# Optimization experiments

Measured on AMD Instinct MI355X. Metric: run time of the kernel, lower is better.

Reference implementation:

```python
import jax, jax.numpy as jnp
import numpy as np

MAT_MODE = [(0, 1), (0, 2), (1, 2)]   # plane axes per component (TensoRF VM)
VEC_MODE = [2, 1, 0]                  # line axis per component
DISTANCE_SCALE = 1.0
WHITE_BG = True


def _bilinear(plane, uv):
    """plane: [C,H,W]; uv: [P,2] in [-1,1] (uv[:,0]->W, uv[:,1]->H). align_corners=True."""
    H, W = plane.shape[-2], plane.shape[-1]
    x = (uv[:, 0] + 1.0) * 0.5 * (W - 1)
    y = (uv[:, 1] + 1.0) * 0.5 * (H - 1)
    x0 = jnp.clip(jnp.floor(x), 0, W - 2).astype(jnp.int32)
    y0 = jnp.clip(jnp.floor(y), 0, H - 2).astype(jnp.int32)
    wx = x - x0
    wy = y - y0
    v00 = plane[:, y0, x0]
    v01 = plane[:, y0, x0 + 1]
    v10 = plane[:, y0 + 1, x0]
    v11 = plane[:, y0 + 1, x0 + 1]
    top = v00 * (1 - wx) + v01 * wx
    bot = v10 * (1 - wx) + v11 * wx
    return top * (1 - wy) + bot * wy   # [C,P]


def _linear1d(line, t):
    """line: [C,L]; t: [P] in [-1,1]. align_corners=True."""
    L = line.shape[-1]
    x = (t + 1.0) * 0.5 * (L - 1)
    x0 = jnp.clip(jnp.floor(x), 0, L - 2).astype(jnp.int32)
    w = x - x0
    return line[:, x0] * (1 - w) + line[:, x0 + 1] * w   # [C,P]


def setup_inputs() -> dict:
    key = jax.random.key(0)
    ks = jax.random.split(key, 8)
    N_rays = 4096
    # camera origins on a sphere of radius 4, dirs aimed at points inside the box
    o = jax.random.normal(ks[0], (N_rays, 3), jnp.float32)
    o = o / jnp.linalg.norm(o, axis=-1, keepdims=True) * 4.0
    tgt = jax.random.uniform(ks[1], (N_rays, 3), jnp.float32, -0.5, 0.5)
    d = tgt - o
    d = d / jnp.linalg.norm(d, axis=-1, keepdims=True)
    rays = jnp.concatenate([o, d], axis=-1)
    return {
        "rays": rays,
        "density_plane": 0.1 * jax.random.normal(ks[2], (3, 16, 256, 256), jnp.float32),
        "density_line": 0.1 * jax.random.normal(ks[3], (3, 16, 256), jnp.float32),
        "app_plane": 0.1 * jax.random.normal(ks[4], (3, 24, 256, 256), jnp.float32),
        "app_line": 0.1 * jax.random.normal(ks[5], (3, 24, 256), jnp.float32),
        "basis_mat": 0.1 * jax.random.normal(ks[6], (72, 3), jnp.float32),
        "aabb": jnp.array([[-1.5, -1.5, -1.5], [1.5, 1.5, 1.5]], jnp.float32),
        "N_samples": 256,
    }


def reference(rays, density_plane, density_line, app_plane, app_line, basis_mat, aabb, N_samples):
    N = rays.shape[0]
    o, d = rays[:, :3], rays[:, 3:6]
    # ray / aabb intersection
    vec = jnp.where(jnp.abs(d) < 1e-6, 1e-6, d)
    rate_a = (aabb[1] - o) / vec
    rate_b = (aabb[0] - o) / vec
    t_min = jnp.clip(jnp.minimum(rate_a, rate_b).max(-1), 0.05)
    t_max = jnp.maximum(jnp.maximum(rate_a, rate_b).min(-1), t_min + 1e-3)
    s = jnp.linspace(0.0, 1.0, N_samples, dtype=jnp.float32)
    z = t_min[:, None] * (1.0 - s) + t_max[:, None] * s          # [N,S]
    dists = jnp.diff(z, axis=-1)
    dists = jnp.concatenate([dists, dists[:, -1:]], axis=-1)      # [N,S]
    pts = o[:, None, :] + d[:, None, :] * z[..., None]            # [N,S,3]
    coords = (pts - aabb[0]) / (aabb[1] - aabb[0]) * 2.0 - 1.0
    inside = jnp.all(jnp.abs(coords) <= 1.0, axis=-1)             # [N,S]
    cf = coords.reshape(-1, 3)                                    # [P,3]

    sigma_feat = 0.0
    app_feats = []
    for i in range(3):
        uv = cf[:, list(MAT_MODE[i])]
        w = cf[:, VEC_MODE[i]]
        sigma_feat = sigma_feat + (_bilinear(density_plane[i], uv) * _linear1d(density_line[i], w)).sum(0)
        app_feats.append(_bilinear(app_plane[i], uv) * _linear1d(app_line[i], w))
    app = jnp.concatenate(app_feats, axis=0).T                    # [P, 72]

    sigma = jax.nn.softplus(sigma_feat).reshape(N, -1) * inside   # [N,S]
    alpha = 1.0 - jnp.exp(-sigma * dists * DISTANCE_SCALE)        # [N,S]
    T = jnp.cumprod(1.0 - alpha + 1e-10, axis=-1)
    T = jnp.concatenate([jnp.ones_like(T[:, :1]), T[:, :-1]], axis=-1)
    weights = alpha * T                                           # [N,S]

    rgb = jax.nn.sigmoid(app @ basis_mat).reshape(N, -1, 3)       # [N,S,3]
    rgb_map = (weights[..., None] * rgb).sum(1)                   # [N,3]
    acc = weights.sum(-1)
    if WHITE_BG:
        rgb_map = rgb_map + (1.0 - acc)[..., None]
    rgb_map = jnp.clip(rgb_map, 0.0, 1.0)
    depth_map = (weights * z).sum(-1, keepdims=True)              # [N,1]
    return rgb_map, depth_map
```

## Files before the change

### kernel.cpp

```cpp
#include <hip/hip_runtime.h>
#include <hip/hip_fp16.h>
#include <cmath>

#define NRAYS 4096
#define NSAMP 256
#define NSAMPLES_TOT (NRAYS * NSAMP)

static constexpr size_t DPT_B = 0;
static constexpr size_t DLT_B = 3145728;
static constexpr size_t APT_B = DLT_B + 24576;
static constexpr size_t ALT_B = APT_B + 4718592;
static constexpr size_t SMP_B = ALT_B + 18432;
static constexpr size_t RAY_B = SMP_B + 8388608;
static constexpr size_t WS_NEED = RAY_B + 131072;

typedef _Float16 __attribute__((ext_vector_type(2))) v2h;
typedef __attribute__((ext_vector_type(2))) float f32x2;

struct u96 { unsigned x, y, z; };

__device__ __forceinline__ u96 ld12(const void* p) {
  u96 v;
  __builtin_memcpy(&v, p, 12);
  return v;
}

__device__ __forceinline__ float dot2acc(__half2 a, __half2 b, float c) {
  return __builtin_amdgcn_fdot2(__builtin_bit_cast(v2h, a),
                                __builtin_bit_cast(v2h, b), c, false);
}

__device__ __forceinline__ __half2 lerp2(__half2 a, __half2 b, __half2 w) {
  return __hfma2(w, __hsub2(b, a), a);
}

__device__ __forceinline__ void ld8h(const __half* p, __half2 h[4]) {
  uint4 r = *(const uint4*)p;
  h[0] = __builtin_bit_cast(__half2, r.x);
  h[1] = __builtin_bit_cast(__half2, r.y);
  h[2] = __builtin_bit_cast(__half2, r.z);
  h[3] = __builtin_bit_cast(__half2, r.w);
}

__device__ __forceinline__ unsigned pack2h(float a, float b) {
  return __builtin_bit_cast(unsigned, __floats2half2_rn(a, b));
}

__device__ __forceinline__ void dec4f8h(unsigned w, __half2& h0, __half2& h1) {
  f32x2 lo = __builtin_amdgcn_cvt_pk_f32_fp8((int)w, false);
  f32x2 hi = __builtin_amdgcn_cvt_pk_f32_fp8((int)w, true);
  h0 = __floats2half2_rn(lo.x, lo.y);
  h1 = __floats2half2_rn(hi.x, hi.y);
}

__device__ __forceinline__ void dec8f8(uint2 q, __half2 h[4]) {
  dec4f8h(q.x, h[0], h[1]);
  dec4f8h(q.y, h[2], h[3]);
}

__device__ __forceinline__ void dec12f8(u96 q, __half2 h[6]) {
  dec4f8h(q.x, h[0], h[1]);
  dec4f8h(q.y, h[2], h[3]);
  dec4f8h(q.z, h[4], h[5]);
}

__device__ __forceinline__ unsigned pk4f8(float a, float b, float c, float d) {
  int w = __builtin_amdgcn_cvt_pk_fp8_f32(a, b, 0, false);
  w = __builtin_amdgcn_cvt_pk_fp8_f32(c, d, w, true);
  return (unsigned)w;
}

__device__ __forceinline__ void grid_uv(float c, int& i0, float& w) {
  float f = (c + 1.0f) * 127.5f;
  float fl = floorf(f);
  fl = fminf(fmaxf(fl, 0.0f), 254.0f);
  i0 = (int)fl;
  w = f - fl;
}

__device__ __forceinline__ void bilin_w(float wx, float wy, __half2& W00,
                                        __half2& W01, __half2& W10, __half2& W11) {
  float ix = 1.0f - wx, iy = 1.0f - wy;
  W00 = __float2half2_rn(ix * iy);
  W01 = __float2half2_rn(wx * iy);
  W10 = __float2half2_rn(ix * wy);
  W11 = __float2half2_rn(wx * wy);
}

__global__ __launch_bounds__(256) void prep_kernel(
    const float* __restrict__ dp, const float* __restrict__ ap,
    const float* __restrict__ dl, const float* __restrict__ al,
    const float* __restrict__ rays, const float* __restrict__ aabb,
    unsigned char* __restrict__ dpt, unsigned char* __restrict__ apt,
    __half* __restrict__ dlt, unsigned char* __restrict__ alt,
    float4* __restrict__ rd) {
  __shared__ float tile[24][257];
  int b = blockIdx.x, x = threadIdx.x;
  if (b < 768) {
    int i = b >> 8, y = b & 255;
    const float* src = dp + (size_t)(i * 16) * 65536 + y * 256;
#pragma unroll
    for (int c = 0; c < 16; ++c) tile[c][x] = src[c * 65536 + x];
    __syncthreads();
    float f[16];
#pragma unroll
    for (int c = 0; c < 16; ++c) f[c] = tile[c][x];
    uint4 v;
    v.x = pk4f8(f[0], f[1], f[2], f[3]);
    v.y = pk4f8(f[4], f[5], f[6], f[7]);
    v.z = pk4f8(f[8], f[9], f[10], f[11]);
    v.w = pk4f8(f[12], f[13], f[14], f[15]);
    *(uint4*)(dpt + ((size_t)(i << 16) + (y << 8) + x) * 16) = v;
  } else if (b < 1536) {
    int t = b - 768;
    int i = t >> 8, y = t & 255;
    const float* src = ap + (size_t)(i * 24) * 65536 + y * 256;
#pragma unroll
    for (int c = 0; c < 24; ++c) tile[c][x] = src[c * 65536 + x];
    __syncthreads();
    float f[24];
#pragma unroll
    for (int c = 0; c < 24; ++c) f[c] = tile[c][x];
    unsigned* dst = (unsigned*)(apt + ((size_t)(i << 16) + (y << 8) + x) * 24);
#pragma unroll
    for (int k = 0; k < 6; ++k)
      dst[k] = pk4f8(f[k * 4], f[k * 4 + 1], f[k * 4 + 2], f[k * 4 + 3]);
  } else if (b < 1539) {
    int i = b - 1536, l = x;
    float f[16];
#pragma unroll
    for (int c = 0; c < 16; ++c) f[c] = dl[(i * 16 + c) * 256 + l];
    uint4 v0, v1;
    v0.x = pack2h(f[0], f[1]);   v0.y = pack2h(f[2], f[3]);
    v0.z = pack2h(f[4], f[5]);   v0.w = pack2h(f[6], f[7]);
    v1.x = pack2h(f[8], f[9]);   v1.y = pack2h(f[10], f[11]);
    v1.z = pack2h(f[12], f[13]); v1.w = pack2h(f[14], f[15]);
    uint4* dst = (uint4*)(dlt + (i * 256 + l) * 16);
    dst[0] = v0; dst[1] = v1;
  } else if (b < 1542) {
    int i = b - 1539, l = x;
    float f[24];
#pragma unroll
    for (int c = 0; c < 24; ++c) f[c] = al[(i * 24 + c) * 256 + l];
    unsigned* dst = (unsigned*)(alt + (i * 256 + l) * 24);
#pragma unroll
    for (int k = 0; k < 6; ++k)
      dst[k] = pk4f8(f[k * 4], f[k * 4 + 1], f[k * 4 + 2], f[k * 4 + 3]);
  } else {
    int r = (b - 1542) * 256 + x;
    if (r < NRAYS) {
      float o0 = rays[r * 6 + 0], o1 = rays[r * 6 + 1], o2 = rays[r * 6 + 2];
      float d0 = rays[r * 6 + 3], d1 = rays[r * 6 + 4], d2 = rays[r * 6 + 5];
      float A0 = aabb[0], A1 = aabb[1], A2 = aabb[2];
      float B0 = aabb[3], B1 = aabb[4], B2 = aabb[5];
      float v0 = fabsf(d0) < 1e-6f ? 1e-6f : d0;
      float v1 = fabsf(d1) < 1e-6f ? 1e-6f : d1;
      float v2 = fabsf(d2) < 1e-6f ? 1e-6f : d2;
      float ra0 = (B0 - o0) / v0, rb0 = (A0 - o0) / v0;
      float ra1 = (B1 - o1) / v1, rb1 = (A1 - o1) / v1;
      float ra2 = (B2 - o2) / v2, rb2 = (A2 - o2) / v2;
      float tmin = fmaxf(fmaxf(fminf(ra0, rb0), fminf(ra1, rb1)), fminf(ra2, rb2));
      tmin = fmaxf(tmin, 0.05f);
      float tmax = fminf(fminf(fmaxf(ra0, rb0), fmaxf(ra1, rb1)), fmaxf(ra2, rb2));
      tmax = fmaxf(tmax, tmin + 0.001f);
      float dt = (tmax - tmin) * (1.0f / 255.0f);
      float s0 = 2.0f / (B0 - A0), s1 = 2.0f / (B1 - A1), s2 = 2.0f / (B2 - A2);
      float4 a2, b2;
      a2.x = (o0 - A0) * s0 - 1.0f; a2.y = (o1 - A1) * s1 - 1.0f;
      a2.z = (o2 - A2) * s2 - 1.0f; a2.w = tmin;
      b2.x = d0 * s0; b2.y = d1 * s1; b2.z = d2 * s2; b2.w = dt;
      rd[r * 2] = a2;
      rd[r * 2 + 1] = b2;
    }
  }
}

__device__ __forceinline__ float density_f8(const unsigned char* __restrict__ pl,
                                            const __half* __restrict__ ln,
                                            int x0, int y0, int l0,
                                            __half2 W00, __half2 W01,
                                            __half2 W10, __half2 W11,
                                            __half2 wl, int sub, float acc) {
  const unsigned char* p = pl + (size_t)((y0 * 256 + x0) << 4) + sub * 8;
  uint2 q00 = *(const uint2*)p;
  uint2 q01 = *(const uint2*)(p + 16);
  uint2 q10 = *(const uint2*)(p + 4096);
  uint2 q11 = *(const uint2*)(p + 4096 + 16);
  __half2 A[4], B[4], C[4], D[4], la[4], lb[4];
  dec8f8(q00, A); dec8f8(q01, B); dec8f8(q10, C); dec8f8(q11, D);
  const __half* lp = ln + (l0 << 4) + sub * 8;
  ld8h(lp, la); ld8h(lp + 16, lb);
#pragma unroll
  for (int r = 0; r < 4; ++r) {
    __half2 m = __hmul2(W00, A[r]);
    m = __hfma2(W01, B[r], m);
    m = __hfma2(W10, C[r], m);
    m = __hfma2(W11, D[r], m);
    __half2 l = lerp2(la[r], lb[r], wl);
    acc = dot2acc(m, l, acc);
  }
  return acc;
}

__device__ __forceinline__ void app_f8(const unsigned char* __restrict__ pl,
                                       const unsigned char* __restrict__ ln,
                                       const __half2* __restrict__ btR,
                                       const __half2* __restrict__ btG,
                                       const __half2* __restrict__ btB,
                                       int x0, int y0, int l0,
                                       __half2 W00, __half2 W01,
                                       __half2 W10, __half2 W11,
                                       __half2 wl, int sub,
                                       float& dr, float& dg, float& db) {
  const unsigned char* p = pl + (size_t)(y0 * 256 + x0) * 24 + sub * 12;
  u96 qA = ld12(p);
  u96 qB = ld12(p + 24);
  u96 qC = ld12(p + 6144);
  u96 qD = ld12(p + 6144 + 24);
  const unsigned char* lp = ln + l0 * 24 + sub * 12;
  u96 qLA = ld12(lp);
  u96 qLB = ld12(lp + 24);
  __half2 A[6], B[6], C[6], D[6], LA[6], LB[6];
  dec12f8(qA, A); dec12f8(qB, B); dec12f8(qC, C); dec12f8(qD, D);
  dec12f8(qLA, LA); dec12f8(qLB, LB);
#pragma unroll
  for (int r = 0; r < 6; ++r) {
    __half2 m = __hmul2(W00, A[r]);
    m = __hfma2(W01, B[r], m);
    m = __hfma2(W10, C[r], m);
    m = __hfma2(W11, D[r], m);
    __half2 l = lerp2(LA[r], LB[r], wl);
    __half2 av = __hmul2(m, l);
    dr = dot2acc(av, btR[r], dr);
    dg = dot2acc(av, btG[r], dg);
    db = dot2acc(av, btB[r], db);
  }
}

__global__ __launch_bounds__(256) void sample_kernel(
    const float4* __restrict__ rd, const float* __restrict__ basis,
    const unsigned char* __restrict__ dpt, const __half* __restrict__ dlt,
    const unsigned char* __restrict__ apt, const unsigned char* __restrict__ alt,
    uint2* __restrict__ smp) {
  __shared__ __align__(16) __half bth[3][3][24];
  int tid = threadIdx.x;
  if (tid < 216) {
    int k = tid / 72, rem = tid - k * 72;
    int m = rem / 24, c = rem - m * 24;
    bth[k][m][c] = __float2half(basis[(m * 24 + c) * 3 + k]);
  }
  __syncthreads();

  int ray = blockIdx.x >> 1;
  int j = ((blockIdx.x & 1) << 7) + (tid >> 1);
  int sub = tid & 1;

  float4 ra = rd[ray * 2];
  float4 rb = rd[ray * 2 + 1];
  float z = fmaf((float)j, rb.w, ra.w);
  float c0 = fmaf(rb.x, z, ra.x);
  float c1 = fmaf(rb.y, z, ra.y);
  float c2 = fmaf(rb.z, z, ra.z);
  bool inside = (fabsf(c0) <= 1.0f) && (fabsf(c1) <= 1.0f) && (fabsf(c2) <= 1.0f);

  float sig = 0.f, dr = 0.f, dg = 0.f, db = 0.f;
  if (inside) {
    int i0, i1, i2;
    float w0, w1, w2;
    grid_uv(c0, i0, w0);
    grid_uv(c1, i1, w1);
    grid_uv(c2, i2, w2);
    __half2 h0 = __float2half2_rn(w0);
    __half2 h1 = __float2half2_rn(w1);
    __half2 h2 = __float2half2_rn(w2);
    __half2 Wa00, Wa01, Wa10, Wa11;
    __half2 Wb00, Wb01, Wb10, Wb11;
    __half2 Wc00, Wc01, Wc10, Wc11;
    bilin_w(w0, w1, Wa00, Wa01, Wa10, Wa11);
    bilin_w(w0, w2, Wb00, Wb01, Wb10, Wb11);
    bilin_w(w1, w2, Wc00, Wc01, Wc10, Wc11);

    sig = density_f8(dpt + 0 * 1048576, dlt + 0 * 4096, i0, i1, i2,
                     Wa00, Wa01, Wa10, Wa11, h2, sub, sig);
    sig = density_f8(dpt + 1 * 1048576, dlt + 1 * 4096, i0, i2, i1,
                     Wb00, Wb01, Wb10, Wb11, h1, sub, sig);
    sig = density_f8(dpt + 2 * 1048576, dlt + 2 * 4096, i1, i2, i0,
                     Wc00, Wc01, Wc10, Wc11, h0, sub, sig);
    app_f8(apt + 0 * 1572864, alt + 0 * 6144,
           (const __half2*)&bth[0][0][sub * 12], (const __half2*)&bth[1][0][sub * 12],
           (const __half2*)&bth[2][0][sub * 12], i0, i1, i2,
           Wa00, Wa01, Wa10, Wa11, h2, sub, dr, dg, db);
    app_f8(apt + 1 * 1572864, alt + 1 * 6144,
           (const __half2*)&bth[0][1][sub * 12], (const __half2*)&bth[1][1][sub * 12],
           (const __half2*)&bth[2][1][sub * 12], i0, i2, i1,
           Wb00, Wb01, Wb10, Wb11, h1, sub, dr, dg, db);
    app_f8(apt + 2 * 1572864, alt + 2 * 6144,
           (const __half2*)&bth[0][2][sub * 12], (const __half2*)&bth[1][2][sub * 12],
           (const __half2*)&bth[2][2][sub * 12], i1, i2, i0,
           Wc00, Wc01, Wc10, Wc11, h0, sub, dr, dg, db);
  }
  sig += __shfl_xor(sig, 1, 64);
  dr += __shfl_xor(dr, 1, 64);
  dg += __shfl_xor(dg, 1, 64);
  db += __shfl_xor(db, 1, 64);

  if (sub == 0) {
    float sp = fmaxf(sig, 0.f) + log1pf(expf(-fabsf(sig)));
    float alpha = inside ? (1.0f - expf(-sp * rb.w)) : 0.0f;
    float cr = 1.0f / (1.0f + expf(-dr));
    float cg = 1.0f / (1.0f + expf(-dg));
    float cb = 1.0f / (1.0f + expf(-db));
    uint2 sv;
    sv.x = pack2h(alpha, cr);
    sv.y = pack2h(cg, cb);
    smp[ray * 256 + j] = sv;
  }
}

__global__ __launch_bounds__(256) void scan_kernel(
    const float4* __restrict__ rd, const uint2* __restrict__ smp,
    float* __restrict__ out) {
  int tid = threadIdx.x;
  int lane = tid & 63;
  int ray = blockIdx.x * 4 + (tid >> 6);

  float tmin = rd[ray * 2].w;
  float dt = rd[ray * 2 + 1].w;

  float C = 1.0f;
  float racc = 0.f, gacc = 0.f, bacc = 0.f, wsum = 0.f, dsum = 0.f;

  for (int q = 0; q < 4; ++q) {
    int j = q * 64 + lane;
    uint2 sv = smp[ray * 256 + j];
    float2 ar = __half22float2(__builtin_bit_cast(__half2, sv.x));
    float2 gb = __half22float2(__builtin_bit_cast(__half2, sv.y));
    float alpha = ar.x;
    float z = fmaf((float)j, dt, tmin);

    float p = 1.0f - alpha + 1e-10f;
#pragma unroll
    for (int off = 1; off < 64; off <<= 1) {
      float t = __shfl_up(p, off, 64);
      if (lane >= off) p *= t;
    }
    float tot = __shfl(p, 63, 64);
    float e = __shfl_up(p, 1, 64);
    if (lane == 0) e = 1.0f;
    float Tj = C * e;
    float w = alpha * Tj;
    racc += w * ar.y;
    gacc += w * gb.x;
    bacc += w * gb.y;
    wsum += w;
    dsum += w * z;
    C *= tot;
  }

#pragma unroll
  for (int off = 32; off > 0; off >>= 1) {
    racc += __shfl_down(racc, off, 64);
    gacc += __shfl_down(gacc, off, 64);
    bacc += __shfl_down(bacc, off, 64);
    wsum += __shfl_down(wsum, off, 64);
    dsum += __shfl_down(dsum, off, 64);
  }
  if (lane == 0) {
    float bgw = 1.0f - wsum;
    out[ray * 3 + 0] = fminf(fmaxf(racc + bgw, 0.f), 1.f);
    out[ray * 3 + 1] = fminf(fmaxf(gacc + bgw, 0.f), 1.f);
    out[ray * 3 + 2] = fminf(fmaxf(bacc + bgw, 0.f), 1.f);
    out[NRAYS * 3 + ray] = dsum;
  }
}

__device__ __forceinline__ float density_orig(const float* __restrict__ plane,
                                              const float* __restrict__ line,
                                              float cx, float cy, float cw) {
  int x0, y0, l0; float wx, wy, wl;
  grid_uv(cx, x0, wx); grid_uv(cy, y0, wy); grid_uv(cw, l0, wl);
  int base = y0 * 256 + x0;
  float s = 0.0f;
#pragma unroll 4
  for (int c = 0; c < 16; ++c) {
    const float* pc = plane + c * 65536;
    float v00 = pc[base], v01 = pc[base + 1];
    float v10 = pc[base + 256], v11 = pc[base + 257];
    float top = fmaf(wx, v01 - v00, v00);
    float bot = fmaf(wx, v11 - v10, v10);
    float mid = fmaf(wy, bot - top, top);
    float la = line[c * 256 + l0], lb = line[c * 256 + l0 + 1];
    float lv = fmaf(wl, lb - la, la);
    s += mid * lv;
  }
  return s;
}

__device__ __forceinline__ void app_orig(const float* __restrict__ plane,
                                         const float* __restrict__ line,
                                         const float* __restrict__ btR,
                                         const float* __restrict__ btG,
                                         const float* __restrict__ btB,
                                         float cx, float cy, float cw,
                                         float& dr, float& dg, float& db) {
  int x0, y0, l0; float wx, wy, wl;
  grid_uv(cx, x0, wx); grid_uv(cy, y0, wy); grid_uv(cw, l0, wl);
  int base = y0 * 256 + x0;
#pragma unroll 4
  for (int c = 0; c < 24; ++c) {
    const float* pc = plane + c * 65536;
    float v00 = pc[base], v01 = pc[base + 1];
    float v10 = pc[base + 256], v11 = pc[base + 257];
    float top = fmaf(wx, v01 - v00, v00);
    float bot = fmaf(wx, v11 - v10, v10);
    float mid = fmaf(wy, bot - top, top);
    float la = line[c * 256 + l0], lb = line[c * 256 + l0 + 1];
    float lv = fmaf(wl, lb - la, la);
    float av = mid * lv;
    dr += av * btR[c]; dg += av * btG[c]; db += av * btB[c];
  }
}

__global__ __launch_bounds__(256) void render_fallback(
    const float* __restrict__ rays, const float* __restrict__ basis,
    const float* __restrict__ aabb, const float* __restrict__ dplane,
    const float* __restrict__ dline, const float* __restrict__ aplane,
    const float* __restrict__ aline, float* __restrict__ out) {
  __shared__ float bt[3 * 72];
  int tid = threadIdx.x;
  if (tid < 216) {
    int k = tid / 72, r = tid - k * 72;
    bt[tid] = basis[r * 3 + k];
  }
  __syncthreads();
  int lane = tid & 63;
  int ray = blockIdx.x * 4 + (tid >> 6);

  float o0 = rays[ray * 6 + 0], o1 = rays[ray * 6 + 1], o2 = rays[ray * 6 + 2];
  float d0 = rays[ray * 6 + 3], d1 = rays[ray * 6 + 4], d2 = rays[ray * 6 + 5];
  float A0 = aabb[0], A1 = aabb[1], A2 = aabb[2];
  float B0 = aabb[3], B1 = aabb[4], B2 = aabb[5];
  float v0 = fabsf(d0) < 1e-6f ? 1e-6f : d0;
  float v1 = fabsf(d1) < 1e-6f ? 1e-6f : d1;
  float v2 = fabsf(d2) < 1e-6f ? 1e-6f : d2;
  float ra0 = (B0 - o0) / v0, rb0 = (A0 - o0) / v0;
  float ra1 = (B1 - o1) / v1, rb1 = (A1 - o1) / v1;
  float ra2 = (B2 - o2) / v2, rb2 = (A2 - o2) / v2;
  float tmin = fmaxf(fmaxf(fminf(ra0, rb0), fminf(ra1, rb1)), fminf(ra2, rb2));
  tmin = fmaxf(tmin, 0.05f);
  float tmax = fminf(fminf(fmaxf(ra0, rb0), fmaxf(ra1, rb1)), fmaxf(ra2, rb2));
  tmax = fmaxf(tmax, tmin + 0.001f);
  float dt = (tmax - tmin) * (1.0f / 255.0f);
  float s0 = 2.0f / (B0 - A0), s1 = 2.0f / (B1 - A1), s2 = 2.0f / (B2 - A2);

  float C = 1.0f;
  float racc = 0.f, gacc = 0.f, bacc = 0.f, wsum = 0.f, dsum = 0.f;
  for (int q = 0; q < 4; ++q) {
    int j = q * 64 + lane;
    float sfrac = (float)j * (1.0f / 255.0f);
    float z = tmin * (1.0f - sfrac) + tmax * sfrac;
    float c0 = (o0 + d0 * z - A0) * s0 - 1.0f;
    float c1 = (o1 + d1 * z - A1) * s1 - 1.0f;
    float c2 = (o2 + d2 * z - A2) * s2 - 1.0f;
    bool inside = (fabsf(c0) <= 1.0f) && (fabsf(c1) <= 1.0f) && (fabsf(c2) <= 1.0f);
    float alpha = 0.f, cr = 0.f, cg = 0.f, cb = 0.f;
    if (inside) {
      float sig = 0.f, dr = 0.f, dg = 0.f, db = 0.f;
      sig += density_orig(dplane + 0 * 1048576, dline + 0 * 4096, c0, c1, c2);
      sig += density_orig(dplane + 1 * 1048576, dline + 1 * 4096, c0, c2, c1);
      sig += density_orig(dplane + 2 * 1048576, dline + 2 * 4096, c1, c2, c0);
      app_orig(aplane + 0 * 1572864, aline + 0 * 6144,
               &bt[0 * 72 + 0], &bt[1 * 72 + 0], &bt[2 * 72 + 0],
               c0, c1, c2, dr, dg, db);
      app_orig(aplane + 1 * 1572864, aline + 1 * 6144,
               &bt[0 * 72 + 24], &bt[1 * 72 + 24], &bt[2 * 72 + 24],
               c0, c2, c1, dr, dg, db);
      app_orig(aplane + 2 * 1572864, aline + 2 * 6144,
               &bt[0 * 72 + 48], &bt[1 * 72 + 48], &bt[2 * 72 + 48],
               c1, c2, c0, dr, dg, db);
      float sp = fmaxf(sig, 0.f) + log1pf(expf(-fabsf(sig)));
      alpha = 1.0f - expf(-sp * dt);
      cr = 1.0f / (1.0f + expf(-dr));
      cg = 1.0f / (1.0f + expf(-dg));
      cb = 1.0f / (1.0f + expf(-db));
    }
    float p = 1.0f - alpha + 1e-10f;
#pragma unroll
    for (int off = 1; off < 64; off <<= 1) {
      float t = __shfl_up(p, off, 64);
      if (lane >= off) p *= t;
    }
    float tot = __shfl(p, 63, 64);
    float e = __shfl_up(p, 1, 64);
    if (lane == 0) e = 1.0f;
    float Tj = C * e;
    float w = alpha * Tj;
    racc += w * cr; gacc += w * cg; bacc += w * cb;
    wsum += w; dsum += w * z;
    C *= tot;
  }
#pragma unroll
  for (int off = 32; off > 0; off >>= 1) {
    racc += __shfl_down(racc, off, 64);
    gacc += __shfl_down(gacc, off, 64);
    bacc += __shfl_down(bacc, off, 64);
    wsum += __shfl_down(wsum, off, 64);
    dsum += __shfl_down(dsum, off, 64);
  }
  if (lane == 0) {
    float bgw = 1.0f - wsum;
    out[ray * 3 + 0] = fminf(fmaxf(racc + bgw, 0.f), 1.f);
    out[ray * 3 + 1] = fminf(fmaxf(gacc + bgw, 0.f), 1.f);
    out[ray * 3 + 2] = fminf(fmaxf(bacc + bgw, 0.f), 1.f);
    out[NRAYS * 3 + ray] = dsum;
  }
}

extern "C" void kernel_launch(void* const* d_in, const int* in_sizes, int n_in,
                              void* d_out, int out_size, void* d_ws, size_t ws_size,
                              hipStream_t stream) {
  const float* rays  = (const float*)d_in[0];
  const float* dp    = (const float*)d_in[1];
  const float* dl    = (const float*)d_in[2];
  const float* ap    = (const float*)d_in[3];
  const float* al    = (const float*)d_in[4];
  const float* basis = (const float*)d_in[5];
  const float* aabb  = (const float*)d_in[6];
  float* out = (float*)d_out;

  if (ws_size >= WS_NEED) {
    char* ws = (char*)d_ws;
    unsigned char* dpt = (unsigned char*)(ws + DPT_B);
    __half* dlt = (__half*)(ws + DLT_B);
    unsigned char* apt = (unsigned char*)(ws + APT_B);
    unsigned char* alt = (unsigned char*)(ws + ALT_B);
    uint2* smp = (uint2*)(ws + SMP_B);
    float4* rayd = (float4*)(ws + RAY_B);
    prep_kernel<<<1558, 256, 0, stream>>>(dp, ap, dl, al, rays, aabb,
                                          dpt, apt, dlt, alt, rayd);
    sample_kernel<<<NRAYS * 2, 256, 0, stream>>>(rayd, basis, dpt, dlt, apt, alt, smp);
    scan_kernel<<<NRAYS / 4, 256, 0, stream>>>(rayd, smp, out);
  } else {
    render_fallback<<<NRAYS / 4, 256, 0, stream>>>(
        rays, basis, aabb, dp, dl, ap, al, out);
  }
}
```

Before: 165.2 us.

## Pad appearance fp8 tables to 32 bytes, use native fp8->f16 convert and fast math

Pads the per-texel appearance plane and line fp8 records from 24 to 32 bytes so each half-thread can fetch its 16 channels with one aligned 16-byte load instead of unaligned 12-byte loads. The basis table in shared memory is zero-padded to match, and the loops cover 8 half2 pairs, of which the last two are zero. Where the compiler offers it, fp8 decode uses the direct scaled fp8->f16 pack-convert rather than going through f32. The epilogue swaps in fast exp, log and rcp intrinsics. The cost is about a third more plane memory traffic and footprint, plus wasted arithmetic on the padding lanes.

```diff
diff --git a/kernel.cpp b/kernel.cpp
--- a/kernel.cpp
+++ b/kernel.cpp
@@ -9,21 +9,22 @@
 static constexpr size_t DPT_B = 0;
 static constexpr size_t DLT_B = 3145728;
 static constexpr size_t APT_B = DLT_B + 24576;
-static constexpr size_t ALT_B = APT_B + 4718592;
-static constexpr size_t SMP_B = ALT_B + 18432;
+static constexpr size_t ALT_B = APT_B + 6291456;
+static constexpr size_t SMP_B = ALT_B + 24576;
 static constexpr size_t RAY_B = SMP_B + 8388608;
 static constexpr size_t WS_NEED = RAY_B + 131072;
 
 typedef _Float16 __attribute__((ext_vector_type(2))) v2h;
 typedef __attribute__((ext_vector_type(2))) float f32x2;
 
-struct u96 { unsigned x, y, z; };
-
-__device__ __forceinline__ u96 ld12(const void* p) {
-  u96 v;
-  __builtin_memcpy(&v, p, 12);
-  return v;
-}
+#if defined(__has_builtin)
+#if __has_builtin(__builtin_amdgcn_cvt_scalef32_pk_f16_fp8)
+#define HAS_SCVT 1
+#endif
+#endif
+#ifndef HAS_SCVT
+#define HAS_SCVT 0
+#endif
 
 __device__ __forceinline__ float dot2acc(__half2 a, __half2 b, float c) {
   return __builtin_amdgcn_fdot2(__builtin_bit_cast(v2h, a),
@@ -47,10 +48,17 @@
 }
 
 __device__ __forceinline__ void dec4f8h(unsigned w, __half2& h0, __half2& h1) {
+#if HAS_SCVT
+  v2h a = __builtin_amdgcn_cvt_scalef32_pk_f16_fp8((int)w, 1.0f, false);
+  v2h b = __builtin_amdgcn_cvt_scalef32_pk_f16_fp8((int)w, 1.0f, true);
+  h0 = __builtin_bit_cast(__half2, a);
+  h1 = __builtin_bit_cast(__half2, b);
+#else
   f32x2 lo = __builtin_amdgcn_cvt_pk_f32_fp8((int)w, false);
   f32x2 hi = __builtin_amdgcn_cvt_pk_f32_fp8((int)w, true);
   h0 = __floats2half2_rn(lo.x, lo.y);
   h1 = __floats2half2_rn(hi.x, hi.y);
+#endif
 }
 
 __device__ __forceinline__ void dec8f8(uint2 q, __half2 h[4]) {
@@ -58,10 +66,11 @@
   dec4f8h(q.y, h[2], h[3]);
 }
 
-__device__ __forceinline__ void dec12f8(u96 q, __half2 h[6]) {
+__device__ __forceinline__ void dec16f8(uint4 q, __half2 h[8]) {
   dec4f8h(q.x, h[0], h[1]);
   dec4f8h(q.y, h[2], h[3]);
   dec4f8h(q.z, h[4], h[5]);
+  dec4f8h(q.w, h[6], h[7]);
 }
 
 __device__ __forceinline__ unsigned pk4f8(float a, float b, float c, float d) {
@@ -121,10 +130,16 @@
     float f[24];
 #pragma unroll
     for (int c = 0; c < 24; ++c) f[c] = tile[c][x];
-    unsigned* dst = (unsigned*)(apt + ((size_t)(i << 16) + (y << 8) + x) * 24);
-#pragma unroll
-    for (int k = 0; k < 6; ++k)
-      dst[k] = pk4f8(f[k * 4], f[k * 4 + 1], f[k * 4 + 2], f[k * 4 + 3]);
+    uint4 v0, v1;
+    v0.x = pk4f8(f[0], f[1], f[2], f[3]);
+    v0.y = pk4f8(f[4], f[5], f[6], f[7]);
+    v0.z = pk4f8(f[8], f[9], f[10], f[11]);
+    v0.w = pk4f8(f[12], f[13], f[14], f[15]);
+    v1.x = pk4f8(f[16], f[17], f[18], f[19]);
+    v1.y = pk4f8(f[20], f[21], f[22], f[23]);
+    v1.z = 0u; v1.w = 0u;
+    uint4* dst = (uint4*)(apt + ((size_t)(i << 16) + (y << 8) + x) * 32);
+    dst[0] = v0; dst[1] = v1;
   } else if (b < 1539) {
     int i = b - 1536, l = x;
     float f[16];
@@ -142,10 +157,16 @@
     float f[24];
 #pragma unroll
     for (int c = 0; c < 24; ++c) f[c] = al[(i * 24 + c) * 256 + l];
-    unsigned* dst = (unsigned*)(alt + (i * 256 + l) * 24);
-#pragma unroll
-    for (int k = 0; k < 6; ++k)
-      dst[k] = pk4f8(f[k * 4], f[k * 4 + 1], f[k * 4 + 2], f[k * 4 + 3]);
+    uint4 v0, v1;
+    v0.x = pk4f8(f[0], f[1], f[2], f[3]);
+    v0.y = pk4f8(f[4], f[5], f[6], f[7]);
+    v0.z = pk4f8(f[8], f[9], f[10], f[11]);
+    v0.w = pk4f8(f[12], f[13], f[14], f[15]);
+    v1.x = pk4f8(f[16], f[17], f[18], f[19]);
+    v1.y = pk4f8(f[20], f[21], f[22], f[23]);
+    v1.z = 0u; v1.w = 0u;
+    uint4* dst = (uint4*)(alt + (i * 256 + l) * 32);
+    dst[0] = v0; dst[1] = v1;
   } else {
     int r = (b - 1542) * 256 + x;
     if (r < NRAYS) {
@@ -212,19 +233,19 @@
                                        __half2 W10, __half2 W11,
                                        __half2 wl, int sub,
                                        float& dr, float& dg, float& db) {
-  const unsigned char* p = pl + (size_t)(y0 * 256 + x0) * 24 + sub * 12;
-  u96 qA = ld12(p);
-  u96 qB = ld12(p + 24);
-  u96 qC = ld12(p + 6144);
-  u96 qD = ld12(p + 6144 + 24);
-  const unsigned char* lp = ln + l0 * 24 + sub * 12;
-  u96 qLA = ld12(lp);
-  u96 qLB = ld12(lp + 24);
-  __half2 A[6], B[6], C[6], D[6], LA[6], LB[6];
-  dec12f8(qA, A); dec12f8(qB, B); dec12f8(qC, C); dec12f8(qD, D);
-  dec12f8(qLA, LA); dec12f8(qLB, LB);
-#pragma unroll
-  for (int r = 0; r < 6; ++r) {
+  const unsigned char* p = pl + ((size_t)(y0 * 256 + x0) << 5) + sub * 16;
+  uint4 qA = *(const uint4*)p;
+  uint4 qB = *(const uint4*)(p + 32);
+  uint4 qC = *(const uint4*)(p + 8192);
+  uint4 qD = *(const uint4*)(p + 8192 + 32);
+  const unsigned char* lp = ln + (l0 << 5) + sub * 16;
+  uint4 qLA = *(const uint4*)lp;
+  uint4 qLB = *(const uint4*)(lp + 32);
+  __half2 A[8], B[8], C[8], D[8], LA[8], LB[8];
+  dec16f8(qA, A); dec16f8(qB, B); dec16f8(qC, C); dec16f8(qD, D);
+  dec16f8(qLA, LA); dec16f8(qLB, LB);
+#pragma unroll
+  for (int r = 0; r < 8; ++r) {
     __half2 m = __hmul2(W00, A[r]);
     m = __hfma2(W01, B[r], m);
     m = __hfma2(W10, C[r], m);
@@ -242,12 +263,13 @@
     const unsigned char* __restrict__ dpt, const __half* __restrict__ dlt,
     const unsigned char* __restrict__ apt, const unsigned char* __restrict__ alt,
     uint2* __restrict__ smp) {
-  __shared__ __align__(16) __half bth[3][3][24];
+  __shared__ __align__(16) __half bth[3][3][32];
   int tid = threadIdx.x;
-  if (tid < 216) {
-    int k = tid / 72, rem = tid - k * 72;
-    int m = rem / 24, c = rem - m * 24;
-    bth[k][m][c] = __float2half(basis[(m * 24 + c) * 3 + k]);
+  for (int t = tid; t < 288; t += 256) {
+    int k = t / 96, rem = t - k * 96;
+    int m = rem >> 5, c = rem & 31;
+    float v = (c < 24) ? basis[(m * 24 + c) * 3 + k] : 0.0f;
+    bth[k][m][c] = __float2half(v);
   }
   __syncthreads();
 
@@ -286,17 +308,17 @@
                      Wb00, Wb01, Wb10, Wb11, h1, sub, sig);
     sig = density_f8(dpt + 2 * 1048576, dlt + 2 * 4096, i1, i2, i0,
                      Wc00, Wc01, Wc10, Wc11, h0, sub, sig);
-    app_f8(apt + 0 * 1572864, alt + 0 * 6144,
-           (const __half2*)&bth[0][0][sub * 12], (const __half2*)&bth[1][0][sub * 12],
-           (const __half2*)&bth[2][0][sub * 12], i0, i1, i2,
+    app_f8(apt + 0 * 2097152, alt + 0 * 8192,
+           (const __half2*)&bth[0][0][sub * 16], (const __half2*)&bth[1][0][sub * 16],
+           (const __half2*)&bth[2][0][sub * 16], i0, i1, i2,
            Wa00, Wa01, Wa10, Wa11, h2, sub, dr, dg, db);
-    app_f8(apt + 1 * 1572864, alt + 1 * 6144,
-           (const __half2*)&bth[0][1][sub * 12], (const __half2*)&bth[1][1][sub * 12],
-           (const __half2*)&bth[2][1][sub * 12], i0, i2, i1,
+    app_f8(apt + 1 * 2097152, alt + 1 * 8192,
+           (const __half2*)&bth[0][1][sub * 16], (const __half2*)&bth[1][1][sub * 16],
+           (const __half2*)&bth[2][1][sub * 16], i0, i2, i1,
            Wb00, Wb01, Wb10, Wb11, h1, sub, dr, dg, db);
-    app_f8(apt + 2 * 1572864, alt + 2 * 6144,
-           (const __half2*)&bth[0][2][sub * 12], (const __half2*)&bth[1][2][sub * 12],
-           (const __half2*)&bth[2][2][sub * 12], i1, i2, i0,
+    app_f8(apt + 2 * 2097152, alt + 2 * 8192,
+           (const __half2*)&bth[0][2][sub * 16], (const __half2*)&bth[1][2][sub * 16],
+           (const __half2*)&bth[2][2][sub * 16], i1, i2, i0,
            Wc00, Wc01, Wc10, Wc11, h0, sub, dr, dg, db);
   }
   sig += __shfl_xor(sig, 1, 64);
@@ -305,11 +327,12 @@
   db += __shfl_xor(db, 1, 64);
 
   if (sub == 0) {
-    float sp = fmaxf(sig, 0.f) + log1pf(expf(-fabsf(sig)));
-    float alpha = inside ? (1.0f - expf(-sp * rb.w)) : 0.0f;
-    float cr = 1.0f / (1.0f + expf(-dr));
-    float cg = 1.0f / (1.0f + expf(-dg));
-    float cb = 1.0f / (1.0f + expf(-db));
+    float e = __expf(-fabsf(sig));
+    float sp = fmaxf(sig, 0.f) + __logf(1.0f + e);
+    float alpha = inside ? (1.0f - __expf(-sp * rb.w)) : 0.0f;
+    float cr = __builtin_amdgcn_rcpf(1.0f + __expf(-dr));
+    float cg = __builtin_amdgcn_rcpf(1.0f + __expf(-dg));
+    float cb = __builtin_amdgcn_rcpf(1.0f + __expf(-db));
     uint2 sv;
     sv.x = pack2h(alpha, cr);
     sv.y = pack2h(cg, cb);
```

New measurement: 153.7 us. 7.0% less time.
